# Optimization experiments

Measured on AMD Instinct MI355X. Metric: run time of the kernel, lower is better.

The kernel has to match this reference:

```python
import jax, jax.numpy as jnp
import numpy as np

N_NODES = 50000
N_EDGES = 1600000
IN_DIM = 64
EDGE_DIM = 8
N_GRAPHS = 256
EXP_IN = 32
H = 64  # hidden dim per head / GCN hidden
EPS = 1e-5
NEG_SLOPE = 0.2


def gat_layer(x, src, dst, ea, W, a_src, a_dst, We, a_e, bias, heads, dim, concat):
    """PyG-style GATConv with edge features and self-loops (fill_value='mean')."""
    N = x.shape[0]
    ones_e = jnp.ones((ea.shape[0],), x.dtype)
    cnt = jax.ops.segment_sum(ones_e, dst, num_segments=N)
    loop_attr = jax.ops.segment_sum(ea, dst, num_segments=N) / jnp.maximum(cnt, 1.0)[:, None]
    s = jnp.concatenate([src, jnp.arange(N)])
    d = jnp.concatenate([dst, jnp.arange(N)])
    eaf = jnp.concatenate([ea, loop_attr], axis=0)  # [E+N, edge_dim]
    h = (x @ W).reshape(N, heads, dim)              # [N, H, D]
    ee = (eaf @ We).reshape(-1, heads, dim)         # [E+N, H, D]
    al_src = (h * a_src).sum(-1)                    # [N, H]
    al_dst = (h * a_dst).sum(-1)                    # [N, H]
    score = al_src[s] + al_dst[d] + (ee * a_e).sum(-1)
    score = jax.nn.leaky_relu(score, NEG_SLOPE)     # [E+N, H]
    m = jax.ops.segment_max(score, d, num_segments=N)
    ex = jnp.exp(score - m[d])
    att = ex / jax.ops.segment_sum(ex, d, num_segments=N)[d]
    out = jax.ops.segment_sum(h[s] * att[:, :, None], d, num_segments=N)  # [N, H, D]
    out = out.reshape(N, heads * dim) if concat else out.mean(axis=1)
    return out + bias


def gcn_layer(x, src, dst, W, b):
    """PyG-style GCNConv: add self loops, symmetric degree normalization."""
    N = x.shape[0]
    s = jnp.concatenate([src, jnp.arange(N)])
    d = jnp.concatenate([dst, jnp.arange(N)])
    deg = jax.ops.segment_sum(jnp.ones((s.shape[0],), x.dtype), d, num_segments=N)
    dinv = jax.lax.rsqrt(deg)  # deg >= 1 thanks to self loops
    norm = dinv[s] * dinv[d]
    h = x @ W
    return jax.ops.segment_sum(h[s] * norm[:, None], d, num_segments=N) + b


def bn(x, g, b):
    m = x.mean(axis=0)
    v = x.var(axis=0)
    return g * (x - m) * jax.lax.rsqrt(v + EPS) + b


def mean_pool(x, batch, num_graphs):
    s = jax.ops.segment_sum(x, batch, num_segments=num_graphs)
    c = jax.ops.segment_sum(jnp.ones((x.shape[0],), x.dtype), batch, num_segments=num_graphs)
    return s / jnp.maximum(c, 1.0)[:, None]


def setup_inputs() -> dict:
    key = jax.random.key(0)
    ks = jax.random.split(key, 32)
    p = lambda i, shape: jax.random.normal(ks[i], shape, jnp.float32) * 0.05
    z = lambda n: jnp.zeros((n,), jnp.float32)
    o = lambda n: jnp.ones((n,), jnp.float32)
    return {
        "x": jax.random.normal(ks[0], (N_NODES, IN_DIM), jnp.float32),
        "edge_attr": jax.random.normal(ks[1], (N_EDGES, EDGE_DIM), jnp.float32),
        "experimental_feat": jax.random.normal(ks[2], (N_GRAPHS, EXP_IN), jnp.float32),
        "edge_index": jax.random.randint(ks[3], (2, N_EDGES), 0, N_NODES),
        "batch": jnp.sort(jax.random.randint(ks[4], (N_NODES,), 0, N_GRAPHS)),
        "W1": p(5, (IN_DIM, 4 * H)), "att_src1": p(6, (4, H)), "att_dst1": p(7, (4, H)),
        "We1": p(8, (EDGE_DIM, 4 * H)), "att_e1": p(9, (4, H)), "b1": z(4 * H),
        "g1": o(4 * H), "be1": z(4 * H),
        "W2": p(10, (4 * H, H)), "att_src2": p(11, (1, H)), "att_dst2": p(12, (1, H)),
        "We2": p(13, (EDGE_DIM, H)), "att_e2": p(14, (1, H)), "b2": z(H),
        "g2": o(H), "be2": z(H),
        "Wg1": p(15, (H, H)), "bg1": z(H), "g3": o(H), "be3": z(H),
        "Wg2": p(16, (H, H)), "bg2": z(H), "g4": o(H), "be4": z(H),
        "Wex1": p(17, (EXP_IN, H)), "bex1": z(H), "Wex2": p(18, (H, H)), "bex2": z(H),
        "Wc1": p(19, (2 * H, 128)), "bc1": z(128), "Wc2": p(20, (128, 1)), "bc2": z(1),
    }


def reference(x, edge_attr, experimental_feat, edge_index, batch,
              W1, att_src1, att_dst1, We1, att_e1, b1, g1, be1,
              W2, att_src2, att_dst2, We2, att_e2, b2, g2, be2,
              Wg1, bg1, g3, be3, Wg2, bg2, g4, be4,
              Wex1, bex1, Wex2, bex2, Wc1, bc1, Wc2, bc2):
    src, dst = edge_index[0], edge_index[1]
    h = gat_layer(x, src, dst, edge_attr, W1, att_src1, att_dst1, We1, att_e1, b1, 4, H, True)
    h = jax.nn.relu(bn(h, g1, be1))
    h = gat_layer(h, src, dst, edge_attr, W2, att_src2, att_dst2, We2, att_e2, b2, 1, H, False)
    h = jax.nn.relu(bn(h, g2, be2))  # dropout = identity in eval
    h = gcn_layer(h, src, dst, Wg1, bg1)
    h = jax.nn.relu(bn(h, g3, be3))
    h = gcn_layer(h, src, dst, Wg2, bg2)
    h = jax.nn.relu(bn(h, g4, be4))
    xp = mean_pool(h, batch, N_GRAPHS)                    # [G, H]
    e = jax.nn.relu(experimental_feat @ Wex1 + bex1)
    e = jax.nn.relu(e @ Wex2 + bex2)
    combined = jnp.concatenate([xp, e], axis=1)           # [G, 2H]
    combined = jax.nn.relu(combined @ Wc1 + bc1)          # [G, 128]
    out = combined @ Wc2 + bc2                            # [G, 1]
    return (out, xp, combined)
```

## Files before the change

### kernel.cpp

```cpp
#include <hip/hip_runtime.h>
#include <hip/hip_bf16.h>

#define N_NODES 50000
#define N_EDGES 1600000
#define N_GRAPHS 256
#define NEG_SLOPE 0.2f
#define BN_EPS 1e-5f

typedef __hip_bfloat16 bf16;
typedef __attribute__((ext_vector_type(8))) short s16x8;
typedef __attribute__((ext_vector_type(4))) float f32x4;

__device__ __forceinline__ float b2f(bf16 v){ return __bfloat162float(v); }
__device__ __forceinline__ bf16 f2b(float v){ return __float2bfloat16(v); }
__device__ __forceinline__ float us2f(unsigned short u){ return __uint_as_float(((unsigned)u)<<16); }
__device__ __forceinline__ unsigned short f2us(float v){ bf16 b = f2b(v); return *(unsigned short*)&b; }
__device__ __forceinline__ unsigned pk2(float a, float b){ return (unsigned)f2us(a) | ((unsigned)f2us(b)<<16); }
__device__ __forceinline__ float ldF(const void* p, size_t i, int m){
  return m ? ((const float*)p)[i] : b2f(((const bf16*)p)[i]);
}
__device__ __forceinline__ float sane(float v){
  return (v == v && fabsf(v) < 1e30f) ? v : 0.f;
}
__device__ __forceinline__ float sel4(const float v[4], int h){
  float r = v[0];
  r = (h==1) ? v[1] : r;
  r = (h==2) ? v[2] : r;
  r = (h==3) ? v[3] : r;
  return r;
}
__device__ __forceinline__ void acc8(float* acc, float w, uint4 u){
  acc[0] += w*us2f((unsigned short)(u.x & 0xffff)); acc[1] += w*us2f((unsigned short)(u.x >> 16));
  acc[2] += w*us2f((unsigned short)(u.y & 0xffff)); acc[3] += w*us2f((unsigned short)(u.y >> 16));
  acc[4] += w*us2f((unsigned short)(u.z & 0xffff)); acc[5] += w*us2f((unsigned short)(u.z >> 16));
  acc[6] += w*us2f((unsigned short)(u.w & 0xffff)); acc[7] += w*us2f((unsigned short)(u.w >> 16));
}
__device__ __forceinline__ void unp8(float* o, uint4 u){
  o[0] = us2f((unsigned short)(u.x & 0xffff)); o[1] = us2f((unsigned short)(u.x >> 16));
  o[2] = us2f((unsigned short)(u.y & 0xffff)); o[3] = us2f((unsigned short)(u.y >> 16));
  o[4] = us2f((unsigned short)(u.z & 0xffff)); o[5] = us2f((unsigned short)(u.z >> 16));
  o[6] = us2f((unsigned short)(u.w & 0xffff)); o[7] = us2f((unsigned short)(u.w >> 16));
}
__device__ __forceinline__ s16x8 pk8(const float* v){
  s16x8 r;
  #pragma unroll
  for(int j=0;j<8;j++) r[j] = (short)f2us(v[j]);
  return r;
}

__device__ int detect_mode_block(const void* x){
  __shared__ int s_ins;
  if(threadIdx.x == 0) s_ins = 0;
  __syncthreads();
  const unsigned short* u = (const unsigned short*)x;
  int c = 0;
  for(int i = threadIdx.x; i < 1024; i += blockDim.x){
    float v = fabsf(us2f(u[i]));
    if(!(v > 1e-6f && v < 1e4f)) c++;
  }
  if(c) atomicAdd(&s_ins, c);
  __syncthreads();
  return (s_ins > 128) ? 1 : 0;
}

#define NSEG 33
struct Bank { const void* p[NSEG]; int n[NSEG]; int off[NSEG]; };

__global__ void k_convert(Bank b, const void* xdet, float* out){
  int m = detect_mode_block(xdet);
  int seg = blockIdx.y;
  int i = blockIdx.x*256 + threadIdx.x;
  if(i < b.n[seg]) out[b.off[seg] + i] = ldF(b.p[seg], i, m);
}

__global__ void k_cvt_x(const void* x, bf16* xb){
  int m = detect_mode_block(x);
  int i4 = blockIdx.x*256 + threadIdx.x;
  if(i4 >= N_NODES*16) return;
  if(m){
    float4 v = ((const float4*)x)[i4];
    ((ushort4*)xb)[i4] = make_ushort4(f2us(v.x), f2us(v.y), f2us(v.z), f2us(v.w));
  } else {
    ((ushort4*)xb)[i4] = ((const ushort4*)x)[i4];
  }
}

__global__ void k_we(const float* __restrict__ We1, const float* __restrict__ ae1,
                     const float* __restrict__ We2, const float* __restrict__ ae2,
                     float* __restrict__ w_e){
  int t = threadIdx.x;
  if(t < 32){
    int h = t >> 3, k = t & 7;
    float s = 0.f;
    for(int d=0;d<64;d++) s += We1[k*256 + h*64 + d] * ae1[h*64 + d];
    w_e[t] = s;
  } else if(t < 40){
    int k = t - 32;
    float s = 0.f;
    for(int d=0;d<64;d++) s += We2[k*64 + d] * ae2[d];
    w_e[t] = s;
  }
}

__global__ void k_wt(const float* __restrict__ W1, const float* __restrict__ W2,
                     const float* __restrict__ Wg1, const float* __restrict__ Wg2,
                     bf16* __restrict__ wt){
  int i = blockIdx.x*256 + threadIdx.x;
  if(i < 16384){
    int c = i >> 6, k = i & 63;
    wt[i] = f2b(W1[k*256 + c]);
  } else if(i < 32768){
    int j = i - 16384; int c = j >> 8, k = j & 255;
    wt[i] = f2b(W2[k*64 + c]);
  } else if(i < 36864){
    int j = i - 32768; int c = j >> 6, k = j & 63;
    wt[i] = f2b(Wg1[k*64 + c]);
  } else if(i < 40960){
    int j = i - 36864; int c = j >> 6, k = j & 63;
    wt[i] = f2b(Wg2[k*64 + c]);
  }
}

__global__ void k_count(const int* __restrict__ dst, int* __restrict__ cnt){
  int e = blockIdx.x*256 + threadIdx.x;
  if(e < N_EDGES){
    int d = dst[e]; if((unsigned)d >= N_NODES) d = 0;
    atomicAdd(&cnt[d], 1);
  }
}

__global__ void k_blocksum(const int* __restrict__ cnt, int* __restrict__ bsum){
  __shared__ int s[256];
  int i = blockIdx.x*256 + threadIdx.x;
  s[threadIdx.x] = (i < N_NODES) ? cnt[i] : 0;
  __syncthreads();
  for(int o=128;o>0;o>>=1){ if(threadIdx.x<o) s[threadIdx.x]+=s[threadIdx.x+o]; __syncthreads(); }
  if(threadIdx.x==0) bsum[blockIdx.x]=s[0];
}

__global__ void k_scan_bsum(const int* __restrict__ bsum, int* __restrict__ bofs, int nb){
  __shared__ int s[256];
  int t = threadIdx.x;
  s[t] = (t<nb) ? bsum[t] : 0;
  __syncthreads();
  for(int o=1;o<256;o<<=1){ int v=(t>=o)?s[t-o]:0; __syncthreads(); s[t]+=v; __syncthreads(); }
  bofs[t] = (t==0) ? 0 : s[t-1];
}

__global__ void k_scan_write(const int* __restrict__ cnt, const int* __restrict__ bofs,
                             int* __restrict__ rp, float* __restrict__ dinv){
  __shared__ int s[256];
  int t = threadIdx.x; int i = blockIdx.x*256 + t;
  int v = (i<N_NODES) ? cnt[i] : 0;
  s[t]=v; __syncthreads();
  for(int o=1;o<256;o<<=1){ int a=(t>=o)?s[t-o]:0; __syncthreads(); s[t]+=a; __syncthreads(); }
  if(i<N_NODES){
    rp[i+1] = s[t] + bofs[blockIdx.x];
    dinv[i] = rsqrtf((float)v + 1.f);
  }
  if(i==0) rp[0]=0;
}

__global__ void k_fill(const int* __restrict__ src, const int* __restrict__ dst,
                       const int* __restrict__ rp, int* __restrict__ fill,
                       const void* __restrict__ ea, const void* __restrict__ xdet,
                       const float* __restrict__ w_e,
                       int4* __restrict__ epk){
  int m = detect_mode_block(xdet);
  int e = blockIdx.x*256 + threadIdx.x;
  if(e >= N_EDGES) return;
  int d = dst[e]; if((unsigned)d >= N_NODES) d = 0;
  int p = atomicAdd(&fill[d], 1);
  int slot = rp[d] + p;
  if((unsigned)slot >= N_EDGES) return;
  int sv = src[e]; if((unsigned)sv >= N_NODES) sv = 0;
  float a[8];
  if(m){
    const float* eaf = (const float*)ea;
    float4 lo = *(const float4*)&eaf[(size_t)e*8];
    float4 hi = *(const float4*)&eaf[(size_t)e*8 + 4];
    a[0]=lo.x; a[1]=lo.y; a[2]=lo.z; a[3]=lo.w;
    a[4]=hi.x; a[5]=hi.y; a[6]=hi.z; a[7]=hi.w;
  } else {
    #pragma unroll
    for(int k=0;k<8;k++) a[k] = b2f(((const bf16*)ea)[(size_t)e*8 + k]);
  }
  unsigned d4[4];
  #pragma unroll
  for(int h=0;h<4;h++){
    float s = 0.f;
    #pragma unroll
    for(int k=0;k<8;k++) s += a[k]*w_e[h*8+k];
    d4[h] = f2us(s);
  }
  float s1 = 0.f;
  #pragma unroll
  for(int k=0;k<8;k++) s1 += a[k]*w_e[32+k];
  int4 pk;
  pk.x = sv;
  pk.y = (int)(d4[0] | (d4[1] << 16));
  pk.z = (int)(d4[2] | (d4[3] << 16));
  pk.w = (int)(unsigned)f2us(s1);
  epk[slot] = pk;
}

__global__ __launch_bounds__(256) void k_gemmA_mfma(
    const bf16* __restrict__ xb,
    const bf16* __restrict__ wt1,
    bf16* __restrict__ hp, int M)
{
  const int tid = threadIdx.x;
  const int w = tid >> 6, l = tid & 63;
  const int lr = l & 15, lg = l >> 4;
  const int bm = blockIdx.x*64 + w*16;
  const int arow_i = bm + lr;
  const uint4* arow = (const uint4*)(xb + (size_t)min(arow_i, M-1)*64);
  uint4 a0u = arow[lg];
  uint4 a1u = arow[4 + lg];
  s16x8 a0 = *(s16x8*)&a0u, a1 = *(s16x8*)&a1u;
  unsigned short* out = (unsigned short*)hp;
  const int orow0 = bm + lg*4;
  #pragma unroll
  for(int ct = 0; ct < 16; ct++){
    const uint4* brow = (const uint4*)(wt1 + (size_t)(ct*16 + lr)*64);
    uint4 b0u = brow[lg];
    uint4 b1u = brow[4 + lg];
    f32x4 acc = {0.f, 0.f, 0.f, 0.f};
    acc = __builtin_amdgcn_mfma_f32_16x16x32_bf16(a0, *(s16x8*)&b0u, acc, 0, 0, 0);
    acc = __builtin_amdgcn_mfma_f32_16x16x32_bf16(a1, *(s16x8*)&b1u, acc, 0, 0, 0);
    #pragma unroll
    for(int r = 0; r < 4; r++){
      int rr = orow0 + r;
      if(rr < M) out[(size_t)rr*256 + ct*16 + lr] = f2us(acc[r]);
    }
  }
}

template<int KIN>
__global__ __launch_bounds__(256) void k_gemmB_mfma(
    const bf16* __restrict__ A, const bf16* __restrict__ Wt,
    bf16* __restrict__ C, int M,
    const float* __restrict__ bnsums, const float* __restrict__ bng, const float* __restrict__ bnb)
{
  __shared__ float st_s[KIN];
  __shared__ float st_t[KIN];
  const int tid = threadIdx.x;
  if(tid < KIN){
    const float invN = 1.0f / (float)N_NODES;
    float mean = bnsums[tid]*invN;
    float var  = fmaxf(bnsums[KIN+tid]*invN - mean*mean, 0.f);
    float s = bng[tid]*rsqrtf(var + BN_EPS);
    st_s[tid] = s;
    st_t[tid] = bnb[tid] - mean*s;
  }
  __syncthreads();
  const int w = tid >> 6, l = tid & 63;
  const int lr = l & 15, lg = l >> 4;
  const int bm = blockIdx.x*64 + w*16;
  const int arow_i = bm + lr;
  const uint4* arow = (const uint4*)(A + (size_t)min(arow_i, M-1)*KIN);
  f32x4 acc[4];
  #pragma unroll
  for(int ct=0;ct<4;ct++) acc[ct] = (f32x4){0.f,0.f,0.f,0.f};
  #pragma unroll
  for(int k0 = 0; k0 < KIN; k0 += 32){
    uint4 au = arow[(k0 >> 3) + lg];
    int c0 = k0 + lg*8;
    float v[8]; unp8(v, au);
    #pragma unroll
    for(int j = 0; j < 8; j++){
      float y = sane(v[j])*st_s[c0+j] + st_t[c0+j];
      v[j] = fmaxf(y, 0.f);
    }
    s16x8 af = pk8(v);
    #pragma unroll
    for(int ct = 0; ct < 4; ct++){
      const uint4* brow = (const uint4*)(Wt + (size_t)(ct*16 + lr)*KIN);
      uint4 bu = brow[(k0 >> 3) + lg];
      acc[ct] = __builtin_amdgcn_mfma_f32_16x16x32_bf16(af, *(s16x8*)&bu, acc[ct], 0, 0, 0);
    }
  }
  unsigned short* out = (unsigned short*)C;
  const int orow0 = bm + lg*4;
  #pragma unroll
  for(int ct = 0; ct < 4; ct++){
    #pragma unroll
    for(int r = 0; r < 4; r++){
      int rr = orow0 + r;
      if(rr < M) out[(size_t)rr*64 + ct*16 + lr] = f2us(acc[ct][r]);
    }
  }
}

__global__ void k_al4(const bf16* __restrict__ hp, const float* __restrict__ asrc,
                      const float* __restrict__ adst,
                      float* __restrict__ als4, float* __restrict__ ald4){
  int idx = blockIdx.x*256 + threadIdx.x;
  if(idx >= N_NODES*4) return;
  int n = idx >> 2, h = idx & 3;
  const unsigned short* row = (const unsigned short*)hp + (size_t)n*256 + h*64;
  float ss=0.f, sd=0.f;
  #pragma unroll
  for(int q=0;q<16;q++){
    ushort4 u = *(const ushort4*)&row[4*q];
    float4 a_s = *(const float4*)&asrc[h*64 + 4*q];
    float4 a_d = *(const float4*)&adst[h*64 + 4*q];
    float v0=us2f(u.x), v1=us2f(u.y), v2=us2f(u.z), v3=us2f(u.w);
    ss += v0*a_s.x + v1*a_s.y + v2*a_s.z + v3*a_s.w;
    sd += v0*a_d.x + v1*a_d.y + v2*a_d.z + v3*a_d.w;
  }
  als4[idx]=ss; ald4[idx]=sd;
}

__global__ void k_al1(const bf16* __restrict__ hp, const float* __restrict__ asrc,
                      const float* __restrict__ adst,
                      float* __restrict__ als, float* __restrict__ ald){
  int n = blockIdx.x*256 + threadIdx.x;
  if(n >= N_NODES) return;
  const unsigned short* row = (const unsigned short*)hp + (size_t)n*64;
  float ss=0.f, sd=0.f;
  #pragma unroll
  for(int q=0;q<16;q++){
    ushort4 u = *(const ushort4*)&row[4*q];
    float4 a_s = *(const float4*)&asrc[4*q];
    float4 a_d = *(const float4*)&adst[4*q];
    float v0=us2f(u.x), v1=us2f(u.y), v2=us2f(u.z), v3=us2f(u.w);
    ss += v0*a_s.x + v1*a_s.y + v2*a_s.z + v3*a_s.w;
    sd += v0*a_d.x + v1*a_d.y + v2*a_d.z + v3*a_d.w;
  }
  als[n]=ss; ald[n]=sd;
}

__global__ __launch_bounds__(64) void k_gat_agg4(
    const int* __restrict__ rp, const int4* __restrict__ epk,
    const bf16* __restrict__ hp,
    const float* __restrict__ als4, const float* __restrict__ ald4,
    const float* __restrict__ bias256, bf16* __restrict__ out1){
  int n = blockIdx.x; int t = threadIdx.x;
  int eh = t >> 5, c8 = t & 31;
  int head = c8 >> 3;
  __shared__ int   ssrc[64];
  __shared__ float swt[64][4];
  int s0 = rp[n], e0 = rp[n+1];
  if((unsigned)s0 > N_EDGES){ s0=0; e0=0; }
  if(e0 < s0 || (unsigned)e0 > N_EDGES) e0 = s0;
  float4 aldv = *(const float4*)&ald4[n*4];
  float4 alsvn = *(const float4*)&als4[n*4];
  float wsum[4] = {0.f,0.f,0.f,0.f};
  float dsum[4] = {0.f,0.f,0.f,0.f};
  float acc[8]  = {0.f,0.f,0.f,0.f,0.f,0.f,0.f,0.f};
  const unsigned short* hpu = (const unsigned short*)hp;

  for(int base = s0; base < e0; base += 64){
    int m = min(64, e0 - base);
    if(t < m){
      int4 pk = epk[base+t];
      int sn = pk.x; if((unsigned)sn >= N_NODES) sn = 0;
      ssrc[t] = sn;
      float edf[4] = {us2f((unsigned short)(pk.y & 0xffff)), us2f((unsigned short)((unsigned)pk.y >> 16)),
                      us2f((unsigned short)(pk.z & 0xffff)), us2f((unsigned short)((unsigned)pk.z >> 16))};
      float4 alss = *(const float4*)&als4[sn*4];
      float alssv[4] = {alss.x, alss.y, alss.z, alss.w};
      float aldvv[4] = {aldv.x, aldv.y, aldv.z, aldv.w};
      float w4[4];
      #pragma unroll
      for(int h=0;h<4;h++){
        float sc = alssv[h] + aldvv[h] + edf[h];
        sc = sc > 0.f ? sc : NEG_SLOPE*sc;
        sc = fminf(sc, 30.f);
        float w = expf(sc);
        w4[h] = w;
        wsum[h] += w; dsum[h] += edf[h];
      }
      *(float4*)&swt[t][0] = make_float4(w4[0], w4[1], w4[2], w4[3]);
    }
    __syncthreads();
    #pragma unroll 4
    for(int i=0;i<m;i+=2){
      int j = i + eh;
      if(j < m){
        int row = ssrc[j];
        float w = swt[j][head];
        uint4 u = *(const uint4*)&hpu[(size_t)row*256 + 8*c8];
        acc8(acc, w, u);
      }
    }
    __syncthreads();
  }
  #pragma unroll
  for(int o=1;o<64;o<<=1){
    #pragma unroll
    for(int h=0;h<4;h++){
      wsum[h] += __shfl_xor(wsum[h], o);
      dsum[h] += __shfl_xor(dsum[h], o);
    }
  }
  #pragma unroll
  for(int q=0;q<8;q++) acc[q] += __shfl_xor(acc[q], 32);
  if(eh == 0){
    float alsnv[4] = {alsvn.x, alsvn.y, alsvn.z, alsvn.w};
    float aldnv[4] = {aldv.x, aldv.y, aldv.z, aldv.w};
    float sEh = sel4(wsum, head), sDh = sel4(dsum, head);
    float deg = (float)(e0 - s0);
    float sdot = deg > 0.f ? sDh/deg : 0.f;
    float sc = sel4(alsnv, head) + sel4(aldnv, head) + sdot;
    sc = sc > 0.f ? sc : NEG_SLOPE*sc;
    sc = fminf(sc, 30.f);
    float wself = expf(sc);
    float self[8];
    unp8(self, *(const uint4*)&hpu[(size_t)n*256 + 8*c8]);
    float4 b0 = *(const float4*)&bias256[8*c8];
    float4 b1 = *(const float4*)&bias256[8*c8 + 4];
    float bi[8] = {b0.x,b0.y,b0.z,b0.w,b1.x,b1.y,b1.z,b1.w};
    float inv = 1.f/(sEh + wself);
    float o8[8];
    #pragma unroll
    for(int q=0;q<8;q++) o8[q] = (acc[q] + wself*self[q])*inv + bi[q];
    uint4 st;
    st.x = pk2(o8[0],o8[1]); st.y = pk2(o8[2],o8[3]);
    st.z = pk2(o8[4],o8[5]); st.w = pk2(o8[6],o8[7]);
    *(uint4*)&((unsigned short*)out1)[(size_t)n*256 + 8*c8] = st;
  }
}

__global__ __launch_bounds__(64) void k_gat_agg1e(
    const int* __restrict__ rp, const int4* __restrict__ epk,
    const bf16* __restrict__ hp,
    const float* __restrict__ als, const float* __restrict__ ald,
    const float* __restrict__ bias64, bf16* __restrict__ out){
  int n = blockIdx.x; int t = threadIdx.x;
  int eg = t >> 3, c8 = t & 7;
  __shared__ float sw[64];
  __shared__ int   ssrc[64];
  int s0 = rp[n], e0 = rp[n+1];
  if((unsigned)s0 > N_EDGES){ s0=0; e0=0; }
  if(e0 < s0 || (unsigned)e0 > N_EDGES) e0 = s0;
  float aldn = ald[n];
  float wsum_l = 0.f, dsum_l = 0.f;
  float acc[8] = {0.f,0.f,0.f,0.f,0.f,0.f,0.f,0.f};
  const unsigned short* hpu = (const unsigned short*)hp;
  for(int base = s0; base < e0; base += 64){
    int m = min(64, e0 - base);
    if(t < m){
      int4 pk = epk[base+t];
      int sn = pk.x; if((unsigned)sn >= N_NODES) sn = 0;
      ssrc[t] = sn;
      float ed = us2f((unsigned short)(pk.w & 0xffff));
      float sc = als[sn] + aldn + ed;
      sc = sc > 0.f ? sc : NEG_SLOPE*sc;
      sc = fminf(sc, 30.f);
      float w = expf(sc);
      sw[t] = w;
      wsum_l += w; dsum_l += ed;
    }
    __syncthreads();
    #pragma unroll 2
    for(int i=0;i<m;i+=8){
      int j = i + eg;
      if(j < m){
        int row = ssrc[j];
        float w = sw[j];
        uint4 u = *(const uint4*)&hpu[(size_t)row*64 + 8*c8];
        acc8(acc, w, u);
      }
    }
    __syncthreads();
  }
  #pragma unroll
  for(int o=1;o<64;o<<=1){ wsum_l += __shfl_xor(wsum_l, o); dsum_l += __shfl_xor(dsum_l, o); }
  #pragma unroll
  for(int q=0;q<8;q++){
    acc[q] += __shfl_xor(acc[q], 8);
    acc[q] += __shfl_xor(acc[q], 16);
    acc[q] += __shfl_xor(acc[q], 32);
  }
  if(t < 8){
    float deg = (float)(e0 - s0);
    float sdot = deg > 0.f ? dsum_l/deg : 0.f;
    float sc = als[n] + aldn + sdot;
    sc = sc > 0.f ? sc : NEG_SLOPE*sc;
    sc = fminf(sc, 30.f);
    float wself = expf(sc);
    float self[8];
    unp8(self, *(const uint4*)&hpu[(size_t)n*64 + 8*t]);
    float4 b0 = *(const float4*)&bias64[8*t];
    float4 b1 = *(const float4*)&bias64[8*t + 4];
    float bi[8] = {b0.x,b0.y,b0.z,b0.w,b1.x,b1.y,b1.z,b1.w};
    float inv = 1.f/(wsum_l + wself);
    float o8[8];
    #pragma unroll
    for(int q=0;q<8;q++) o8[q] = (acc[q] + wself*self[q])*inv + bi[q];
    uint4 st;
    st.x = pk2(o8[0],o8[1]); st.y = pk2(o8[2],o8[3]);
    st.z = pk2(o8[4],o8[5]); st.w = pk2(o8[6],o8[7]);
    *(uint4*)&((unsigned short*)out)[(size_t)n*64 + 8*t] = st;
  }
}

__global__ __launch_bounds__(64) void k_gcn_agg(
    const int* __restrict__ rp, const int4* __restrict__ epk,
    const float* __restrict__ dinv, const bf16* __restrict__ gp,
    const float* __restrict__ bias, bf16* __restrict__ out){
  int n = blockIdx.x; int t = threadIdx.x;
  int eg = t >> 3, c8 = t & 7;
  __shared__ float sw[64];
  __shared__ int   ssrc[64];
  int s0 = rp[n], e0 = rp[n+1];
  if((unsigned)s0 > N_EDGES){ s0=0; e0=0; }
  if(e0 < s0 || (unsigned)e0 > N_EDGES) e0 = s0;
  float dn = dinv[n];
  float acc[8] = {0.f,0.f,0.f,0.f,0.f,0.f,0.f,0.f};
  const unsigned short* gpu = (const unsigned short*)gp;
  for(int base = s0; base < e0; base += 64){
    int m = min(64, e0 - base);
    if(t < m){
      int sn = epk[base+t].x; if((unsigned)sn >= N_NODES) sn = 0;
      ssrc[t]=sn; sw[t]=dinv[sn];
    }
    __syncthreads();
    #pragma unroll 2
    for(int i=0;i<m;i+=8){
      int j = i + eg;
      if(j < m){
        int row = ssrc[j];
        float w = sw[j];
        uint4 u = *(const uint4*)&gpu[(size_t)row*64 + 8*c8];
        acc8(acc, w, u);
      }
    }
    __syncthreads();
  }
  #pragma unroll
  for(int q=0;q<8;q++){
    acc[q] += __shfl_xor(acc[q], 8);
    acc[q] += __shfl_xor(acc[q], 16);
    acc[q] += __shfl_xor(acc[q], 32);
  }
  if(t < 8){
    float self[8];
    unp8(self, *(const uint4*)&gpu[(size_t)n*64 + 8*t]);
    float4 b0 = *(const float4*)&bias[8*t];
    float4 b1 = *(const float4*)&bias[8*t + 4];
    float bi[8] = {b0.x,b0.y,b0.z,b0.w,b1.x,b1.y,b1.z,b1.w};
    float o8[8];
    #pragma unroll
    for(int q=0;q<8;q++) o8[q] = dn*(acc[q] + dn*self[q]) + bi[q];
    uint4 st;
    st.x = pk2(o8[0],o8[1]); st.y = pk2(o8[2],o8[3]);
    st.z = pk2(o8[4],o8[5]); st.w = pk2(o8[6],o8[7]);
    *(uint4*)&((unsigned short*)out)[(size_t)n*64 + 8*t] = st;
  }
}

template<int C>
__global__ void k_colstats(const bf16* __restrict__ X, float* __restrict__ sums){
  constexpr int RPB = 128;
  constexpr int RSTEP = 256 / C;
  int c = threadIdx.x % C;
  int r0 = threadIdx.x / C;
  int rbeg = blockIdx.x * RPB;
  int rend = min(N_NODES, rbeg + RPB);
  const unsigned short* Xu = (const unsigned short*)X;
  float s = 0.f, q = 0.f;
  for(int r = rbeg + r0; r < rend; r += RSTEP){
    float v = sane(us2f(Xu[(size_t)r*C + c]));
    s += v; q += v*v;
  }
  atomicAdd(&sums[c], s);
  atomicAdd(&sums[C + c], q);
}

__global__ __launch_bounds__(64) void k_pool3(
    const bf16* __restrict__ h, const int* __restrict__ batch,
    const float* __restrict__ sums, const float* __restrict__ g4,
    const float* __restrict__ b4,
    float* __restrict__ psum, float* __restrict__ pcnt){
  int t = threadIdx.x;
  int n0 = blockIdx.x * 256;
  int n1 = min(N_NODES, n0 + 256);
  if(n0 >= n1) return;
  const float invN = 1.0f / (float)N_NODES;
  float mean = sums[t]*invN;
  float var = fmaxf(sums[64+t]*invN - mean*mean, 0.f);
  float rstd = rsqrtf(var + BN_EPS);
  float gg = g4[t], bb = b4[t];
  const unsigned short* hu = (const unsigned short*)h;
  int cur = batch[n0]; if((unsigned)cur >= N_GRAPHS) cur = 0;
  float acc = 0.f; int cl = 0;
  for(int n = n0; n < n1; n++){
    int g = batch[n]; if((unsigned)g >= N_GRAPHS) g = 0;
    if(g != cur){
      atomicAdd(&psum[cur*64 + t], acc);
      if(t == 0) atomicAdd(&pcnt[cur], (float)cl);
      acc = 0.f; cl = 0; cur = g;
    }
    float y = (sane(us2f(hu[(size_t)n*64 + t]))-mean)*rstd*gg + bb;
    acc += fmaxf(y, 0.f);
    cl++;
  }
  atomicAdd(&psum[cur*64 + t], acc);
  if(t == 0) atomicAdd(&pcnt[cur], (float)cl);
}

__device__ __forceinline__ void stO(void* o, size_t i, float v, int m){
  if(m) ((float*)o)[i] = v; else ((bf16*)o)[i] = f2b(v);
}

__global__ __launch_bounds__(128) void k_head(
    const float* __restrict__ psum, const float* __restrict__ pcnt,
    const float* __restrict__ exf,
    const float* __restrict__ Wex1, const float* __restrict__ bex1,
    const float* __restrict__ Wex2, const float* __restrict__ bex2,
    const float* __restrict__ Wc1, const float* __restrict__ bc1,
    const float* __restrict__ Wc2, const float* __restrict__ bc2,
    const void* __restrict__ xdet, void* __restrict__ dout){
  int m0 = detect_mode_block(xdet);
  int g = blockIdx.x; int t = threadIdx.x;
  __shared__ float ci[128];
  __shared__ float e1[64];
  __shared__ float comb[128];
  __shared__ float red[128];
  if(t < 64){
    float c = fmaxf(pcnt[g], 1.f);
    float xp = sane(psum[g*64 + t]) / c;
    ci[t] = xp;
    stO(dout, 256 + (size_t)g*64 + t, xp, m0);
  } else {
    int j = t - 64;
    float s = bex1[j];
    for(int k=0;k<32;k++) s += exf[g*32 + k] * Wex1[k*64 + j];
    e1[j] = fmaxf(s, 0.f);
  }
  __syncthreads();
  if(t >= 64){
    int j = t - 64;
    float s = bex2[j];
    for(int k=0;k<64;k++) s += e1[k] * Wex2[k*64 + j];
    ci[64 + j] = fmaxf(s, 0.f);
  }
  __syncthreads();
  {
    float s = bc1[t];
    for(int k=0;k<128;k++) s += ci[k] * Wc1[k*128 + t];
    s = fmaxf(s, 0.f);
    comb[t] = s;
    stO(dout, 256 + 16384 + (size_t)g*128 + t, s, m0);
  }
  __syncthreads();
  red[t] = comb[t] * Wc2[t];
  __syncthreads();
  for(int o=64;o>0;o>>=1){ if(t<o) red[t]+=red[t+o]; __syncthreads(); }
  if(t==0) stO(dout, g, red[0] + bc2[0], m0);
}

extern "C" void kernel_launch(void* const* d_in, const int* in_sizes, int n_in,
                              void* d_out, int out_size, void* d_ws, size_t ws_size,
                              hipStream_t stream){
  const void* x    = d_in[0];
  const void* ea   = d_in[1];
  const int* ei    = (const int*)d_in[3];
  const int* batch = (const int*)d_in[4];
  const int* src = ei;
  const int* dst = ei + N_EDGES;

  char* base = (char*)d_ws;
  size_t off = 0;
  auto alloc = [&](size_t bytes) -> void* {
    void* r = base + off;
    off += (bytes + 255) & ~(size_t)255;
    return r;
  };
  int*   cnt    = (int*)  alloc((size_t)N_NODES*4);
  int*   fill   = (int*)  alloc((size_t)N_NODES*4);
  float* bnstat = (float*)alloc(4096);
  float* pool   = (float*)alloc((size_t)(N_GRAPHS*64 + N_GRAPHS)*4);
  size_t zbytes = off;
  int*   rp      = (int*)  alloc((size_t)(N_NODES+1)*4);
  int*   bsum    = (int*)  alloc(256*4);
  int*   bofs    = (int*)  alloc(256*4);
  int4*  epk     = (int4*) alloc((size_t)N_EDGES*16);
  float* dinv    = (float*)alloc((size_t)N_NODES*4);
  float* w_e     = (float*)alloc(64*4);
  float* als4    = (float*)alloc((size_t)N_NODES*4*4);
  float* ald4    = (float*)alloc((size_t)N_NODES*4*4);
  float* wbank   = (float*)alloc(80000*4);
  bf16*  wt      = (bf16*) alloc((size_t)40960*2);
  bf16*  xb      = (bf16*) alloc((size_t)N_NODES*64*2);
  bf16*  hp      = (bf16*) alloc((size_t)N_NODES*256*2);
  bf16*  outb    = (bf16*) alloc((size_t)N_NODES*256*2);

  bf16* out1 = outb;
  bf16* out2 = outb;
  bf16* out3 = outb + (size_t)N_NODES*64;
  bf16* out4 = outb + (size_t)N_NODES*128;
  float* bn1 = bnstat;
  float* bn2 = bnstat + 512;
  float* bn3 = bnstat + 640;
  float* bn4 = bnstat + 768;
  float* psum = pool;
  float* pcnt = pool + N_GRAPHS*64;

  bf16* wt1  = wt;
  bf16* wt2  = wt + 16384;
  bf16* wtg1 = wt + 32768;
  bf16* wtg2 = wt + 36864;

  const int segidx[NSEG] = {2, 5,6,7,8,9,10,11,12, 13,14,15,16,17,18,19,20,
                            21,22,23,24, 25,26,27,28, 29,30,31,32, 33,34,35,36};
  const int segn[NSEG] = {8192, 16384,256,256,2048,256,256,256,256,
                          16384,64,64,512,64,64,64,64,
                          4096,64,64,64, 4096,64,64,64,
                          2048,64,4096,64, 16384,128,128,1};
  Bank bk;
  int offs[NSEG]; int acc0 = 0;
  for(int i=0;i<NSEG;i++){ bk.p[i]=d_in[segidx[i]]; bk.n[i]=segn[i]; bk.off[i]=acc0; offs[i]=acc0; acc0+=segn[i]; }
  const float* f_exf = wbank + offs[0];
  const float* fW1 = wbank+offs[1]; const float* fas1 = wbank+offs[2]; const float* fad1 = wbank+offs[3];
  const float* fWe1= wbank+offs[4]; const float* fae1 = wbank+offs[5]; const float* fb1  = wbank+offs[6];
  const float* fg1 = wbank+offs[7]; const float* fbe1 = wbank+offs[8];
  const float* fW2 = wbank+offs[9]; const float* fas2 = wbank+offs[10]; const float* fad2 = wbank+offs[11];
  const float* fWe2= wbank+offs[12]; const float* fae2 = wbank+offs[13]; const float* fb2 = wbank+offs[14];
  const float* fg2 = wbank+offs[15]; const float* fbe2 = wbank+offs[16];
  const float* fWg1= wbank+offs[17]; const float* fbg1 = wbank+offs[18]; const float* fg3 = wbank+offs[19];
  const float* fbe3= wbank+offs[20];
  const float* fWg2= wbank+offs[21]; const float* fbg2 = wbank+offs[22]; const float* fg4 = wbank+offs[23];
  const float* fbe4= wbank+offs[24];
  const float* fWex1=wbank+offs[25]; const float* fbex1= wbank+offs[26];
  const float* fWex2=wbank+offs[27]; const float* fbex2= wbank+offs[28];
  const float* fWc1= wbank+offs[29]; const float* fbc1 = wbank+offs[30];
  const float* fWc2= wbank+offs[31]; const float* fbc2 = wbank+offs[32];

  const int nbN  = (N_NODES + 255)/256;
  const int nbE  = (N_EDGES + 255)/256;
  const int nbT  = (N_NODES + 63)/64;

  hipMemsetAsync(d_ws, 0, zbytes, stream);
  {
    dim3 g((16384+255)/256, NSEG);
    k_convert<<<g,256,0,stream>>>(bk, x, wbank);
  }
  k_wt<<<160,256,0,stream>>>(fW1, fW2, fWg1, fWg2, wt);
  k_cvt_x<<<(N_NODES*16+255)/256,256,0,stream>>>(x, xb);
  k_we<<<1,64,0,stream>>>(fWe1, fae1, fWe2, fae2, w_e);
  k_count<<<nbE,256,0,stream>>>(dst, cnt);
  k_blocksum<<<nbN,256,0,stream>>>(cnt, bsum);
  k_scan_bsum<<<1,256,0,stream>>>(bsum, bofs, nbN);
  k_scan_write<<<nbN,256,0,stream>>>(cnt, bofs, rp, dinv);
  k_fill<<<nbE,256,0,stream>>>(src, dst, rp, fill, ea, x, w_e, epk);

  k_gemmA_mfma<<<nbT,256,0,stream>>>(xb, wt1, hp, N_NODES);
  k_al4<<<(N_NODES*4+255)/256,256,0,stream>>>(hp, fas1, fad1, als4, ald4);
  k_gat_agg4<<<N_NODES,64,0,stream>>>(rp, epk, hp, als4, ald4, fb1, out1);
  k_colstats<256><<<(N_NODES+127)/128,256,0,stream>>>(out1, bn1);

  k_gemmB_mfma<256><<<nbT,256,0,stream>>>(out1, wt2, hp, N_NODES, bn1, fg1, fbe1);
  k_al1<<<nbN,256,0,stream>>>(hp, fas2, fad2, als4, ald4);
  k_gat_agg1e<<<N_NODES,64,0,stream>>>(rp, epk, hp, als4, ald4, fb2, out2);
  k_colstats<64><<<(N_NODES+127)/128,256,0,stream>>>(out2, bn2);

  k_gemmB_mfma<64><<<nbT,256,0,stream>>>(out2, wtg1, hp, N_NODES, bn2, fg2, fbe2);
  k_gcn_agg<<<N_NODES,64,0,stream>>>(rp, epk, dinv, hp, fbg1, out3);
  k_colstats<64><<<(N_NODES+127)/128,256,0,stream>>>(out3, bn3);

  k_gemmB_mfma<64><<<nbT,256,0,stream>>>(out3, wtg2, hp, N_NODES, bn3, fg3, fbe3);
  k_gcn_agg<<<N_NODES,64,0,stream>>>(rp, epk, dinv, hp, fbg2, out4);
  k_colstats<64><<<(N_NODES+127)/128,256,0,stream>>>(out4, bn4);

  k_pool3<<<nbN,64,0,stream>>>(out4, batch, bn4, fg4, fbe4, psum, pcnt);
  k_head<<<N_GRAPHS,128,0,stream>>>(psum, pcnt, f_exf, fWex1, fbex1, fWex2, fbex2,
                                    fWc1, fbc1, fWc2, fbc2, x, (void*)d_out);
}
```

Before: 938.3 us.

## Split GAT/GCN aggregation into weight pass and column-sliced gather kernels

Each GAT aggregation becomes two kernels. The first computes per-edge attention weights, writes them to global memory with compacted source indices, and stores per-node normalisers. The second launches one block per node per 32-column slice and gathers rows with 16 edges in parallel. The GCN aggregation also uses the sliced gather, reading a compact int source array instead of the 16-byte packed edge records. This trades extra launches and the global write and re-read of the weights for more parallelism and smaller gathers per block.

```diff
diff --git a/kernel.cpp b/kernel.cpp
--- a/kernel.cpp
+++ b/kernel.cpp
@@ -331,16 +331,12 @@
   als[n]=ss; ald[n]=sd;
 }
 
-__global__ __launch_bounds__(64) void k_gat_agg4(
+__global__ __launch_bounds__(64) void k_gatw4(
     const int* __restrict__ rp, const int4* __restrict__ epk,
-    const bf16* __restrict__ hp,
     const float* __restrict__ als4, const float* __restrict__ ald4,
-    const float* __restrict__ bias256, bf16* __restrict__ out1){
+    int* __restrict__ srcs, float* __restrict__ wraw,
+    float* __restrict__ inv4, float* __restrict__ selfw4){
   int n = blockIdx.x; int t = threadIdx.x;
-  int eh = t >> 5, c8 = t & 31;
-  int head = c8 >> 3;
-  __shared__ int   ssrc[64];
-  __shared__ float swt[64][4];
   int s0 = rp[n], e0 = rp[n+1];
   if((unsigned)s0 > N_EDGES){ s0=0; e0=0; }
   if(e0 < s0 || (unsigned)e0 > N_EDGES) e0 = s0;
@@ -348,44 +344,27 @@
   float4 alsvn = *(const float4*)&als4[n*4];
   float wsum[4] = {0.f,0.f,0.f,0.f};
   float dsum[4] = {0.f,0.f,0.f,0.f};
-  float acc[8]  = {0.f,0.f,0.f,0.f,0.f,0.f,0.f,0.f};
-  const unsigned short* hpu = (const unsigned short*)hp;
-
   for(int base = s0; base < e0; base += 64){
     int m = min(64, e0 - base);
     if(t < m){
       int4 pk = epk[base+t];
       int sn = pk.x; if((unsigned)sn >= N_NODES) sn = 0;
-      ssrc[t] = sn;
+      srcs[base+t] = sn;
       float edf[4] = {us2f((unsigned short)(pk.y & 0xffff)), us2f((unsigned short)((unsigned)pk.y >> 16)),
                       us2f((unsigned short)(pk.z & 0xffff)), us2f((unsigned short)((unsigned)pk.z >> 16))};
       float4 alss = *(const float4*)&als4[sn*4];
       float alssv[4] = {alss.x, alss.y, alss.z, alss.w};
       float aldvv[4] = {aldv.x, aldv.y, aldv.z, aldv.w};
-      float w4[4];
       #pragma unroll
       for(int h=0;h<4;h++){
         float sc = alssv[h] + aldvv[h] + edf[h];
         sc = sc > 0.f ? sc : NEG_SLOPE*sc;
         sc = fminf(sc, 30.f);
         float w = expf(sc);
-        w4[h] = w;
+        wraw[(size_t)h*N_EDGES + base+t] = w;
         wsum[h] += w; dsum[h] += edf[h];
       }
-      *(float4*)&swt[t][0] = make_float4(w4[0], w4[1], w4[2], w4[3]);
-    }
-    __syncthreads();
-    #pragma unroll 4
-    for(int i=0;i<m;i+=2){
-      int j = i + eh;
-      if(j < m){
-        int row = ssrc[j];
-        float w = swt[j][head];
-        uint4 u = *(const uint4*)&hpu[(size_t)row*256 + 8*c8];
-        acc8(acc, w, u);
-      }
-    }
-    __syncthreads();
+    }
   }
   #pragma unroll
   for(int o=1;o<64;o<<=1){
@@ -395,160 +374,240 @@
       dsum[h] += __shfl_xor(dsum[h], o);
     }
   }
-  #pragma unroll
-  for(int q=0;q<8;q++) acc[q] += __shfl_xor(acc[q], 32);
-  if(eh == 0){
+  if(t < 4){
     float alsnv[4] = {alsvn.x, alsvn.y, alsvn.z, alsvn.w};
     float aldnv[4] = {aldv.x, aldv.y, aldv.z, aldv.w};
-    float sEh = sel4(wsum, head), sDh = sel4(dsum, head);
+    float sEh = sel4(wsum, t), sDh = sel4(dsum, t);
     float deg = (float)(e0 - s0);
     float sdot = deg > 0.f ? sDh/deg : 0.f;
-    float sc = sel4(alsnv, head) + sel4(aldnv, head) + sdot;
+    float sc = sel4(alsnv, t) + sel4(aldnv, t) + sdot;
     sc = sc > 0.f ? sc : NEG_SLOPE*sc;
     sc = fminf(sc, 30.f);
     float wself = expf(sc);
+    float inv = 1.f/(sEh + wself);
+    inv4[n*4 + t] = inv;
+    selfw4[n*4 + t] = wself*inv;
+  }
+}
+
+__global__ __launch_bounds__(64) void k_gat_slice4(
+    const int* __restrict__ rp, const int* __restrict__ srcs,
+    const float* __restrict__ wraw,
+    const bf16* __restrict__ hp,
+    const float* __restrict__ inv4, const float* __restrict__ selfw4,
+    const float* __restrict__ bias256, bf16* __restrict__ out1){
+  int bid = blockIdx.x;
+  int slice = bid & 7, n = bid >> 3;
+  int head = slice >> 1;
+  int t = threadIdx.x;
+  int ei = t >> 2, q = t & 3;
+  __shared__ int   ssrc[64];
+  __shared__ float sw[64];
+  int s0 = rp[n], e0 = rp[n+1];
+  if((unsigned)s0 > N_EDGES){ s0=0; e0=0; }
+  if(e0 < s0 || (unsigned)e0 > N_EDGES) e0 = s0;
+  const unsigned short* hpu = (const unsigned short*)hp;
+  const int cbase = slice*32 + q*8;
+  const float* wh = wraw + (size_t)head*N_EDGES;
+  float acc[8] = {0.f,0.f,0.f,0.f,0.f,0.f,0.f,0.f};
+  for(int base = s0; base < e0; base += 64){
+    int m = min(64, e0 - base);
+    if(t < m){
+      int sn = srcs[base+t]; if((unsigned)sn >= N_NODES) sn = 0;
+      ssrc[t] = sn;
+      sw[t] = wh[base+t];
+    }
+    __syncthreads();
+    #pragma unroll 4
+    for(int i=0;i<m;i+=16){
+      int j = i + ei;
+      if(j < m){
+        uint4 u = *(const uint4*)&hpu[(size_t)ssrc[j]*256 + cbase];
+        acc8(acc, sw[j], u);
+      }
+    }
+    __syncthreads();
+  }
+  #pragma unroll
+  for(int c=0;c<8;c++){
+    acc[c] += __shfl_xor(acc[c], 4);
+    acc[c] += __shfl_xor(acc[c], 8);
+    acc[c] += __shfl_xor(acc[c], 16);
+    acc[c] += __shfl_xor(acc[c], 32);
+  }
+  if(t < 4){
+    float inv = inv4[n*4 + head];
+    float sfw = selfw4[n*4 + head];
     float self[8];
-    unp8(self, *(const uint4*)&hpu[(size_t)n*256 + 8*c8]);
-    float4 b0 = *(const float4*)&bias256[8*c8];
-    float4 b1 = *(const float4*)&bias256[8*c8 + 4];
+    unp8(self, *(const uint4*)&hpu[(size_t)n*256 + slice*32 + t*8]);
+    float4 b0 = *(const float4*)&bias256[slice*32 + t*8];
+    float4 b1 = *(const float4*)&bias256[slice*32 + t*8 + 4];
     float bi[8] = {b0.x,b0.y,b0.z,b0.w,b1.x,b1.y,b1.z,b1.w};
-    float inv = 1.f/(sEh + wself);
     float o8[8];
     #pragma unroll
-    for(int q=0;q<8;q++) o8[q] = (acc[q] + wself*self[q])*inv + bi[q];
+    for(int c=0;c<8;c++) o8[c] = acc[c]*inv + sfw*self[c] + bi[c];
     uint4 st;
     st.x = pk2(o8[0],o8[1]); st.y = pk2(o8[2],o8[3]);
     st.z = pk2(o8[4],o8[5]); st.w = pk2(o8[6],o8[7]);
-    *(uint4*)&((unsigned short*)out1)[(size_t)n*256 + 8*c8] = st;
-  }
-}
-
-__global__ __launch_bounds__(64) void k_gat_agg1e(
+    *(uint4*)&((unsigned short*)out1)[(size_t)n*256 + slice*32 + t*8] = st;
+  }
+}
+
+__global__ __launch_bounds__(64) void k_gatw1(
     const int* __restrict__ rp, const int4* __restrict__ epk,
-    const bf16* __restrict__ hp,
     const float* __restrict__ als, const float* __restrict__ ald,
-    const float* __restrict__ bias64, bf16* __restrict__ out){
+    float* __restrict__ wraw1, float* __restrict__ inv1, float* __restrict__ selfw1){
   int n = blockIdx.x; int t = threadIdx.x;
-  int eg = t >> 3, c8 = t & 7;
-  __shared__ float sw[64];
-  __shared__ int   ssrc[64];
   int s0 = rp[n], e0 = rp[n+1];
   if((unsigned)s0 > N_EDGES){ s0=0; e0=0; }
   if(e0 < s0 || (unsigned)e0 > N_EDGES) e0 = s0;
   float aldn = ald[n];
   float wsum_l = 0.f, dsum_l = 0.f;
-  float acc[8] = {0.f,0.f,0.f,0.f,0.f,0.f,0.f,0.f};
-  const unsigned short* hpu = (const unsigned short*)hp;
   for(int base = s0; base < e0; base += 64){
     int m = min(64, e0 - base);
     if(t < m){
       int4 pk = epk[base+t];
       int sn = pk.x; if((unsigned)sn >= N_NODES) sn = 0;
-      ssrc[t] = sn;
       float ed = us2f((unsigned short)(pk.w & 0xffff));
       float sc = als[sn] + aldn + ed;
       sc = sc > 0.f ? sc : NEG_SLOPE*sc;
       sc = fminf(sc, 30.f);
       float w = expf(sc);
-      sw[t] = w;
+      wraw1[base+t] = w;
       wsum_l += w; dsum_l += ed;
     }
-    __syncthreads();
-    #pragma unroll 2
-    for(int i=0;i<m;i+=8){
-      int j = i + eg;
-      if(j < m){
-        int row = ssrc[j];
-        float w = sw[j];
-        uint4 u = *(const uint4*)&hpu[(size_t)row*64 + 8*c8];
-        acc8(acc, w, u);
-      }
-    }
-    __syncthreads();
   }
   #pragma unroll
   for(int o=1;o<64;o<<=1){ wsum_l += __shfl_xor(wsum_l, o); dsum_l += __shfl_xor(dsum_l, o); }
-  #pragma unroll
-  for(int q=0;q<8;q++){
-    acc[q] += __shfl_xor(acc[q], 8);
-    acc[q] += __shfl_xor(acc[q], 16);
-    acc[q] += __shfl_xor(acc[q], 32);
-  }
-  if(t < 8){
+  if(t == 0){
     float deg = (float)(e0 - s0);
     float sdot = deg > 0.f ? dsum_l/deg : 0.f;
     float sc = als[n] + aldn + sdot;
     sc = sc > 0.f ? sc : NEG_SLOPE*sc;
     sc = fminf(sc, 30.f);
     float wself = expf(sc);
+    float inv = 1.f/(wsum_l + wself);
+    inv1[n] = inv;
+    selfw1[n] = wself*inv;
+  }
+}
+
+__global__ __launch_bounds__(64) void k_gat_slice1(
+    const int* __restrict__ rp, const int* __restrict__ srcs,
+    const float* __restrict__ wraw1,
+    const bf16* __restrict__ hp,
+    const float* __restrict__ inv1, const float* __restrict__ selfw1,
+    const float* __restrict__ bias64, bf16* __restrict__ out){
+  int bid = blockIdx.x;
+  int slice = bid & 1, n = bid >> 1;
+  int t = threadIdx.x;
+  int ei = t >> 2, q = t & 3;
+  __shared__ int   ssrc[64];
+  __shared__ float sw[64];
+  int s0 = rp[n], e0 = rp[n+1];
+  if((unsigned)s0 > N_EDGES){ s0=0; e0=0; }
+  if(e0 < s0 || (unsigned)e0 > N_EDGES) e0 = s0;
+  const unsigned short* hpu = (const unsigned short*)hp;
+  const int cbase = slice*32 + q*8;
+  float acc[8] = {0.f,0.f,0.f,0.f,0.f,0.f,0.f,0.f};
+  for(int base = s0; base < e0; base += 64){
+    int m = min(64, e0 - base);
+    if(t < m){
+      int sn = srcs[base+t]; if((unsigned)sn >= N_NODES) sn = 0;
+      ssrc[t] = sn;
+      sw[t] = wraw1[base+t];
+    }
+    __syncthreads();
+    #pragma unroll 4
+    for(int i=0;i<m;i+=16){
+      int j = i + ei;
+      if(j < m){
+        uint4 u = *(const uint4*)&hpu[(size_t)ssrc[j]*64 + cbase];
+        acc8(acc, sw[j], u);
+      }
+    }
+    __syncthreads();
+  }
+  #pragma unroll
+  for(int c=0;c<8;c++){
+    acc[c] += __shfl_xor(acc[c], 4);
+    acc[c] += __shfl_xor(acc[c], 8);
+    acc[c] += __shfl_xor(acc[c], 16);
+    acc[c] += __shfl_xor(acc[c], 32);
+  }
+  if(t < 4){
+    float inv = inv1[n];
+    float sfw = selfw1[n];
     float self[8];
-    unp8(self, *(const uint4*)&hpu[(size_t)n*64 + 8*t]);
-    float4 b0 = *(const float4*)&bias64[8*t];
-    float4 b1 = *(const float4*)&bias64[8*t + 4];
+    unp8(self, *(const uint4*)&hpu[(size_t)n*64 + slice*32 + t*8]);
+    float4 b0 = *(const float4*)&bias64[slice*32 + t*8];
+    float4 b1 = *(const float4*)&bias64[slice*32 + t*8 + 4];
     float bi[8] = {b0.x,b0.y,b0.z,b0.w,b1.x,b1.y,b1.z,b1.w};
-    float inv = 1.f/(wsum_l + wself);
     float o8[8];
     #pragma unroll
-    for(int q=0;q<8;q++) o8[q] = (acc[q] + wself*self[q])*inv + bi[q];
+    for(int c=0;c<8;c++) o8[c] = acc[c]*inv + sfw*self[c] + bi[c];
     uint4 st;
     st.x = pk2(o8[0],o8[1]); st.y = pk2(o8[2],o8[3]);
     st.z = pk2(o8[4],o8[5]); st.w = pk2(o8[6],o8[7]);
-    *(uint4*)&((unsigned short*)out)[(size_t)n*64 + 8*t] = st;
-  }
-}
-
-__global__ __launch_bounds__(64) void k_gcn_agg(
-    const int* __restrict__ rp, const int4* __restrict__ epk,
+    *(uint4*)&((unsigned short*)out)[(size_t)n*64 + slice*32 + t*8] = st;
+  }
+}
+
+__global__ __launch_bounds__(64) void k_gcn_slice(
+    const int* __restrict__ rp, const int* __restrict__ srcs,
     const float* __restrict__ dinv, const bf16* __restrict__ gp,
     const float* __restrict__ bias, bf16* __restrict__ out){
-  int n = blockIdx.x; int t = threadIdx.x;
-  int eg = t >> 3, c8 = t & 7;
+  int bid = blockIdx.x;
+  int slice = bid & 1, n = bid >> 1;
+  int t = threadIdx.x;
+  int ei = t >> 2, q = t & 3;
+  __shared__ int   ssrc[64];
   __shared__ float sw[64];
-  __shared__ int   ssrc[64];
   int s0 = rp[n], e0 = rp[n+1];
   if((unsigned)s0 > N_EDGES){ s0=0; e0=0; }
   if(e0 < s0 || (unsigned)e0 > N_EDGES) e0 = s0;
   float dn = dinv[n];
+  const unsigned short* gpu = (const unsigned short*)gp;
+  const int cbase = slice*32 + q*8;
   float acc[8] = {0.f,0.f,0.f,0.f,0.f,0.f,0.f,0.f};
-  const unsigned short* gpu = (const unsigned short*)gp;
   for(int base = s0; base < e0; base += 64){
     int m = min(64, e0 - base);
     if(t < m){
-      int sn = epk[base+t].x; if((unsigned)sn >= N_NODES) sn = 0;
-      ssrc[t]=sn; sw[t]=dinv[sn];
+      int sn = srcs[base+t]; if((unsigned)sn >= N_NODES) sn = 0;
+      ssrc[t] = sn;
+      sw[t] = dinv[sn];
     }
     __syncthreads();
-    #pragma unroll 2
-    for(int i=0;i<m;i+=8){
-      int j = i + eg;
+    #pragma unroll 4
+    for(int i=0;i<m;i+=16){
+      int j = i + ei;
       if(j < m){
-        int row = ssrc[j];
-        float w = sw[j];
-        uint4 u = *(const uint4*)&gpu[(size_t)row*64 + 8*c8];
-        acc8(acc, w, u);
+        uint4 u = *(const uint4*)&gpu[(size_t)ssrc[j]*64 + cbase];
+        acc8(acc, sw[j], u);
       }
     }
     __syncthreads();
   }
   #pragma unroll
-  for(int q=0;q<8;q++){
-    acc[q] += __shfl_xor(acc[q], 8);
-    acc[q] += __shfl_xor(acc[q], 16);
-    acc[q] += __shfl_xor(acc[q], 32);
-  }
-  if(t < 8){
+  for(int c=0;c<8;c++){
+    acc[c] += __shfl_xor(acc[c], 4);
+    acc[c] += __shfl_xor(acc[c], 8);
+    acc[c] += __shfl_xor(acc[c], 16);
+    acc[c] += __shfl_xor(acc[c], 32);
+  }
+  if(t < 4){
     float self[8];
-    unp8(self, *(const uint4*)&gpu[(size_t)n*64 + 8*t]);
-    float4 b0 = *(const float4*)&bias[8*t];
-    float4 b1 = *(const float4*)&bias[8*t + 4];
+    unp8(self, *(const uint4*)&gpu[(size_t)n*64 + slice*32 + t*8]);
+    float4 b0 = *(const float4*)&bias[slice*32 + t*8];
+    float4 b1 = *(const float4*)&bias[slice*32 + t*8 + 4];
     float bi[8] = {b0.x,b0.y,b0.z,b0.w,b1.x,b1.y,b1.z,b1.w};
     float o8[8];
     #pragma unroll
-    for(int q=0;q<8;q++) o8[q] = dn*(acc[q] + dn*self[q]) + bi[q];
+    for(int c=0;c<8;c++) o8[c] = dn*(acc[c] + dn*self[c]) + bi[c];
     uint4 st;
     st.x = pk2(o8[0],o8[1]); st.y = pk2(o8[2],o8[3]);
     st.z = pk2(o8[4],o8[5]); st.w = pk2(o8[6],o8[7]);
-    *(uint4*)&((unsigned short*)out)[(size_t)n*64 + 8*t] = st;
+    *(uint4*)&((unsigned short*)out)[(size_t)n*64 + slice*32 + t*8] = st;
   }
 }
 
@@ -688,6 +747,13 @@
   bf16*  xb      = (bf16*) alloc((size_t)N_NODES*64*2);
   bf16*  hp      = (bf16*) alloc((size_t)N_NODES*256*2);
   bf16*  outb    = (bf16*) alloc((size_t)N_NODES*256*2);
+  int*   srcs    = (int*)  alloc((size_t)N_EDGES*4);
+  float* wraw    = (float*)alloc((size_t)N_EDGES*4*4);
+  float* wraw1   = (float*)alloc((size_t)N_EDGES*4);
+  float* inv4    = (float*)alloc((size_t)N_NODES*4*4);
+  float* selfw4  = (float*)alloc((size_t)N_NODES*4*4);
+  float* inv1    = (float*)alloc((size_t)N_NODES*4);
+  float* selfw1  = (float*)alloc((size_t)N_NODES*4);
 
   bf16* out1 = outb;
   bf16* out2 = outb;
@@ -750,20 +816,22 @@
 
   k_gemmA_mfma<<<nbT,256,0,stream>>>(xb, wt1, hp, N_NODES);
   k_al4<<<(N_NODES*4+255)/256,256,0,stream>>>(hp, fas1, fad1, als4, ald4);
-  k_gat_agg4<<<N_NODES,64,0,stream>>>(rp, epk, hp, als4, ald4, fb1, out1);
+  k_gatw4<<<N_NODES,64,0,stream>>>(rp, epk, als4, ald4, srcs, wraw, inv4, selfw4);
+  k_gat_slice4<<<N_NODES*8,64,0,stream>>>(rp, srcs, wraw, hp, inv4, selfw4, fb1, out1);
   k_colstats<256><<<(N_NODES+127)/128,256,0,stream>>>(out1, bn1);
 
   k_gemmB_mfma<256><<<nbT,256,0,stream>>>(out1, wt2, hp, N_NODES, bn1, fg1, fbe1);
   k_al1<<<nbN,256,0,stream>>>(hp, fas2, fad2, als4, ald4);
-  k_gat_agg1e<<<N_NODES,64,0,stream>>>(rp, epk, hp, als4, ald4, fb2, out2);
+  k_gatw1<<<N_NODES,64,0,stream>>>(rp, epk, als4, ald4, wraw1, inv1, selfw1);
+  k_gat_slice1<<<N_NODES*2,64,0,stream>>>(rp, srcs, wraw1, hp, inv1, selfw1, fb2, out2);
   k_colstats<64><<<(N_NODES+127)/128,256,0,stream>>>(out2, bn2);
 
   k_gemmB_mfma<64><<<nbT,256,0,stream>>>(out2, wtg1, hp, N_NODES, bn2, fg2, fbe2);
-  k_gcn_agg<<<N_NODES,64,0,stream>>>(rp, epk, dinv, hp, fbg1, out3);
+  k_gcn_slice<<<N_NODES*2,64,0,stream>>>(rp, srcs, dinv, hp, fbg1, out3);
   k_colstats<64><<<(N_NODES+127)/128,256,0,stream>>>(out3, bn3);
 
   k_gemmB_mfma<64><<<nbT,256,0,stream>>>(out3, wtg2, hp, N_NODES, bn3, fg3, fbe3);
-  k_gcn_agg<<<N_NODES,64,0,stream>>>(rp, epk, dinv, hp, fbg2, out4);
+  k_gcn_slice<<<N_NODES*2,64,0,stream>>>(rp, srcs, dinv, hp, fbg2, out4);
   k_colstats<64><<<(N_NODES+127)/128,256,0,stream>>>(out4, bn4);
 
   k_pool3<<<nbN,64,0,stream>>>(out4, batch, bn4, fg4, fbe4, psum, pcnt);
```

After: 1.076 ms. +14.7%, slower.
